# Kernel optimization log

Measured on AMD Instinct MI355X. Metric: run time of the kernel, lower is better.

Reference implementation:

```python
import jax, jax.numpy as jnp
import numpy as np

NUM_HEADS = 16
HIDDEN = 1024
HEAD = HIDDEN // NUM_HEADS
NEG_INF = -10000.0


def setup_inputs() -> dict:
    key = jax.random.key(0)
    k1, k2, k3, k4 = jax.random.split(key, 4)
    B, S = 4, 2048
    x = jax.random.normal(k1, (B, S, HIDDEN), dtype=jnp.float32)
    pos_embeds = jax.random.normal(k2, (S, HIDDEN), dtype=jnp.float32)
    # Dense(3*hidden, use_bias=False) and Dense(hidden, use_bias=False)
    Wqkv = jax.random.normal(k3, (HIDDEN, 3 * HIDDEN), dtype=jnp.float32) / np.sqrt(HIDDEN)
    Wo = jax.random.normal(k4, (HIDDEN, HIDDEN), dtype=jnp.float32) / np.sqrt(HIDDEN)
    return {"x": x, "pos_embeds": pos_embeds, "Wqkv": Wqkv, "Wo": Wo}


def _compute_qkv(t, Wqkv):
    # rearrange '... s (k n h) -> k ... n s h', k=3, n=NUM_HEADS
    proj = t @ Wqkv  # [..., s, 3*n*h]
    proj = proj.reshape(*t.shape[:-1], 3, NUM_HEADS, HEAD)  # [..., s, 3, n, h]
    # move: k first, then leading dims, then n, s, h
    nd = proj.ndim
    perm = (nd - 3,) + tuple(range(nd - 4)) + (nd - 2, nd - 4, nd - 1)
    return jnp.transpose(proj, perm)  # [3, ..., n, s, h]


def reference(x, pos_embeds, Wqkv, Wo):
    S = x.shape[-2]
    q, k, v = _compute_qkv(x, Wqkv)  # each [B, n, S, h]
    pos_qkv = _compute_qkv(pos_embeds[:S], Wqkv)  # [3, n, S, h]
    pos_q, pos_k = pos_qkv[0], pos_qkv[1]
    q = q + pos_q  # broadcast over batch
    k = k + pos_k
    scores = jnp.einsum('bnqh,bnkh->bnqk', q, k) / np.sqrt(HEAD).astype(np.float32)
    causal = jnp.arange(S)[:, None] < jnp.arange(S)[None, :]  # strict upper triangle (future)
    scores = jnp.where(causal, NEG_INF, scores)
    probs = jax.nn.softmax(scores, axis=-1)
    # dropout deterministic (training=False) -> identity
    combined = jnp.einsum('bnqk,bnkh->bnqh', probs, v)  # [B, n, S, h]
    combined = jnp.transpose(combined, (0, 2, 1, 3)).reshape(x.shape[0], S, HIDDEN)  # '... n q h -> ... q (n h)'
    out = combined @ Wo
    return out
```

## Files before the change

### kernel.cpp

```cpp
#include <hip/hip_runtime.h>


typedef float f32x4 __attribute__((ext_vector_type(4)));
typedef short bf16x8 __attribute__((ext_vector_type(8)));
typedef short bf16x4 __attribute__((ext_vector_type(4)));

#define MFMA_BF16(a, b, c) __builtin_amdgcn_mfma_f32_16x16x32_bf16((a), (b), (c), 0, 0, 0)

#if __has_builtin(__builtin_amdgcn_mfma_f32_16x16x16bf16_1k)
#define HAVE_MFMA16 1
#define MFMA_BF16_K16(a, b, c) __builtin_amdgcn_mfma_f32_16x16x16bf16_1k((a), (b), (c), 0, 0, 0)
#else
#define HAVE_MFMA16 0
#endif

__device__ __forceinline__ short f2bf(float f) {
  union { float f; unsigned u; } v; v.f = f;
  unsigned u = v.u;
  u += 0x7fffu + ((u >> 16) & 1u);
  return (short)(u >> 16);
}

__device__ __forceinline__ float bf2f(short s) {
  union { unsigned u; float f; } v;
  v.u = ((unsigned)(unsigned short)s) << 16;
  return v.f;
}

__device__ __forceinline__ float fast_exp2(float x) {
#if __has_builtin(__builtin_amdgcn_exp2f)
  return __builtin_amdgcn_exp2f(x);
#else
  return exp2f(x);
#endif
}

__device__ __forceinline__ int cvt_pk_bf16(float lo, float hi) {
  int r;
  asm("v_cvt_pk_bf16_f32 %0, %1, %2" : "=v"(r) : "v"(lo), "v"(hi));
  return r;
}

__device__ __forceinline__ void gl_lds16(const short* g, short* l) {
  __builtin_amdgcn_global_load_lds(
      (const __attribute__((address_space(1))) unsigned*)(g),
      (__attribute__((address_space(3))) unsigned*)(l), 16, 0, 0);
}

__device__ __forceinline__ int swzK(int row, int colbyte) {
  return row * 64 + (((colbyte) ^ ((row & 7) << 4)) >> 1);
}
__device__ __forceinline__ int swz32(int row, int colbyte) {
  return row * 32 + (((colbyte) ^ ((row & 3) << 4)) >> 1);
}
__device__ __forceinline__ int swzV(int row, int colbyte) {
  return row * 64 + ((((colbyte >> 3) + row) & 15) << 2);
}
__device__ __forceinline__ int swzE(int row, int col) {
  return row * 128 + ((((col >> 3) ^ (row & 15)) << 3) | (col & 7));
}

__device__ const int QT_X[30] = {5,6,7,8,9,10,11,11,12,12,13,13,14,14,15,15,
                                 4,10, 3,9,15, 2,8,14, 1,7,13, 0,6,12};
__device__ const int CH_X[30] = {0,0,0,0,0,0,0,1,0,1,0,1,0,1,0,1,
                                 0,1, 0,1,2, 0,1,2, 0,1,2, 0,1,2};
__device__ const int START_QT[16] = {0,1,2,3,4,5,6,8,10,12,14,16,18,21,24,27};

__global__ __launch_bounds__(256) void prep_and_transpose(
    const float* __restrict__ x, const float* __restrict__ pos,
    const float* __restrict__ wqkv, const float* __restrict__ wo,
    short* __restrict__ xb, short* __restrict__ xpb,
    short* __restrict__ outqkv, short* __restrict__ outo) {
  __shared__ float tile[32][33];
  const int n = blockIdx.x;
  if (n < 8192) {
    int i = n * 256 + threadIdx.x;
    int idx = i * 4;
    const float4 xv = *(const float4*)(x + idx);
    const float4 pv = *(const float4*)(pos + (idx & ((2048 * 1024) - 1)));
    short4 a, b;
    a.x = f2bf(xv.x); a.y = f2bf(xv.y); a.z = f2bf(xv.z); a.w = f2bf(xv.w);
    b.x = f2bf(xv.x + pv.x); b.y = f2bf(xv.y + pv.y);
    b.z = f2bf(xv.z + pv.z); b.w = f2bf(xv.w + pv.w);
    *(short4*)(xb + idx) = a;
    *(short4*)(xpb + idx) = b;
    return;
  }
  const int m = n - 8192;
  const int bx = m & 127;
  const int k0 = (m >> 7) * 32;
  const float* __restrict__ in = (bx < 96) ? wqkv : wo;
  short* __restrict__ out = (bx < 96) ? outqkv : outo;
  const int N = (bx < 96) ? 3072 : 1024;
  const int n0 = ((bx < 96) ? bx : (bx - 96)) * 32;
  int c = threadIdx.x & 31, r0 = threadIdx.x >> 5;
  for (int i = 0; i < 4; i++) {
    int r = r0 + i * 8;
    tile[r][c] = in[(size_t)(k0 + r) * N + n0 + c];
  }
  __syncthreads();
  for (int i = 0; i < 4; i++) {
    int r = r0 + i * 8;
    out[(size_t)(n0 + r) * 1024 + k0 + c] = f2bf(tile[c][r]);
  }
}

__global__ __launch_bounds__(256) void gemm_qkv(const short* __restrict__ xb,
                                                const short* __restrict__ xpb,
                                                const short* __restrict__ wt,
                                                short* __restrict__ qg,
                                                short* __restrict__ kg,
                                                short* __restrict__ vtg) {
  __shared__ __align__(16) short Sh[16384];
  const int n = blockIdx.x;
  const int idx = n >> 3;
  const int bm = (n & 7) * 8 + (idx & 7);
  const int bn = idx >> 3;
  const short* __restrict__ A = (bn < 16) ? xpb : xb;
  const int tid = threadIdx.x;
  const int lane = tid & 63, wid = tid >> 6;
  const int wm = wid & 1, wn = wid >> 1;
  const int quad = lane >> 4, l16 = lane & 15;
  const f32x4 fzero = {0.f, 0.f, 0.f, 0.f};
  f32x4 acc[4][4];
  for (int mt = 0; mt < 4; mt++)
    for (int nt = 0; nt < 4; nt++) acc[mt][nt] = fzero;
  const int arow0 = bm * 128, brow0 = bn * 128;

  int prow[2], pcol[2], pbase[2];
#pragma unroll
  for (int i = 0; i < 2; i++) {
    int p = (wid * 2 + i) * 64 + lane;
    prow[i] = p >> 2;
    pcol[i] = ((p & 3) ^ ((p >> 2) & 3)) * 8;
    pbase[i] = (wid * 2 + i) * 512;
  }

#define STAGE_QKV(BUF, K0)                                                    \
  {                                                                           \
    _Pragma("unroll")                                                         \
    for (int i = 0; i < 2; i++) {                                             \
      gl_lds16(A + (size_t)(arow0 + prow[i]) * 1024 + (K0) + pcol[i],         \
               Sh + (BUF)*8192 + pbase[i]);                                   \
      gl_lds16(wt + (size_t)(brow0 + prow[i]) * 1024 + (K0) + pcol[i],        \
               Sh + (BUF)*8192 + 4096 + pbase[i]);                            \
    }                                                                         \
  }

#define COMPUTE_QKV(BASE)                                                     \
  {                                                                           \
    const short* As_ = (BASE);                                                \
    const short* Bs_ = (BASE) + 4096;                                         \
    bf16x8 af[4], bfr[4];                                                     \
    _Pragma("unroll")                                                         \
    for (int mt = 0; mt < 4; mt++)                                            \
      af[mt] = *(const bf16x8*)(As_ + swz32(wm * 64 + mt * 16 + l16, quad * 16)); \
    _Pragma("unroll")                                                         \
    for (int nt = 0; nt < 4; nt++)                                            \
      bfr[nt] = *(const bf16x8*)(Bs_ + swz32(wn * 64 + nt * 16 + l16, quad * 16)); \
    _Pragma("unroll")                                                         \
    for (int mt = 0; mt < 4; mt++)                                            \
      _Pragma("unroll")                                                       \
      for (int nt = 0; nt < 4; nt++)                                          \
        acc[mt][nt] = MFMA_BF16(af[mt], bfr[nt], acc[mt][nt]);                \
  }

  STAGE_QKV(0, 0);
  __syncthreads();
  for (int t = 0; t < 32; t += 2) {
    if (t + 1 < 32) STAGE_QKV(1, (t + 1) * 32);
    COMPUTE_QKV(Sh);
    __syncthreads();
    if (t + 2 < 32) STAGE_QKV(0, (t + 2) * 32);
    COMPUTE_QKV(Sh + 8192);
    __syncthreads();
  }

  short* Sf = Sh;
  const int kk = bn >> 3;
  const int bglob = (bm * 128) >> 11;
  const int s0v = (bm * 128) & 2047;
  if (kk == 2) {
#pragma unroll
    for (int mt = 0; mt < 4; mt++)
#pragma unroll
      for (int nt = 0; nt < 4; nt++) {
        int col = wn * 64 + nt * 16 + l16;
        int sb = wm * 64 + mt * 16 + quad * 4;
        int2 pk;
        pk.x = cvt_pk_bf16(acc[mt][nt][0], acc[mt][nt][1]);
        pk.y = cvt_pk_bf16(acc[mt][nt][2], acc[mt][nt][3]);
        *(int2*)(Sf + swzE(col, sb)) = pk;
      }
    __syncthreads();
    const int col = tid >> 1, half = tid & 1;
    int head = (bn * 2 + (col >> 6)) & 15;
    int hh = col & 63;
    int4* dst = (int4*)(vtg + (size_t)((bglob * 16 + head) * 64 + hh) * 2048 + s0v + half * 64);
#pragma unroll
    for (int c = 0; c < 8; c++)
      dst[c] = *(const int4*)(Sf + swzE(col, half * 64 + c * 8));
  } else {
    const float scale = (kk == 0) ? 0.18033688f : 1.0f;
#pragma unroll
    for (int mt = 0; mt < 4; mt++)
#pragma unroll
      for (int nt = 0; nt < 4; nt++) {
        int col = wn * 64 + nt * 16 + l16;
#pragma unroll
        for (int r = 0; r < 4; r++) {
          int s_loc = wm * 64 + mt * 16 + quad * 4 + r;
          Sf[swzE(s_loc, col)] = f2bf(acc[mt][nt][r] * scale);
        }
      }
    __syncthreads();
    const int row = tid >> 1, half = tid & 1;
    int head = (bn * 2 + half) & 15;
    short* __restrict__ dstp = (kk == 0) ? qg : kg;
    int4* dst = (int4*)(dstp + (size_t)((bglob * 16 + head) * 2048 + s0v + row) * 64);
#pragma unroll
    for (int c = 0; c < 8; c++)
      dst[c] = *(const int4*)(Sf + swzE(row, half * 64 + c * 8));
  }
}

__global__ __launch_bounds__(256, 3) void attn_part(const short* __restrict__ qg,
                                                    const short* __restrict__ kg,
                                                    const short* __restrict__ vtg,
                                                    short* __restrict__ pO,
                                                    float* __restrict__ pL) {
  const int n = blockIdx.x;
  const int i = n >> 3;
  const int bh = (n & 7) * 8 + i / 30;
  const int slot = i % 30;
  const int qt = QT_X[slot], ch = CH_X[slot];
  const int p = bh * 30 + START_QT[qt] + ch;
  const short* __restrict__ Q = qg + (size_t)bh * 2048 * 64;
  const short* __restrict__ K = kg + (size_t)bh * 2048 * 64;
  const short* __restrict__ VT = vtg + (size_t)bh * 64 * 2048;
  __shared__ __align__(16) short KV[2][64 * 64];
  short* Ks = &KV[0][0];
  short* Vs = &KV[1][0];
#if !HAVE_MFMA16
  __shared__ __align__(16) short Ps[4][16 * 72];
#endif
  const int tid = threadIdx.x, lane = tid & 63, w = tid >> 6;
  const int quad = lane >> 4, l16 = lane & 15;
  const f32x4 fzero = {0.f, 0.f, 0.f, 0.f};

  bf16x8 bq[2][2];
#pragma unroll
  for (int sub = 0; sub < 2; sub++) {
    int qrow = qt * 128 + w * 32 + sub * 16 + l16;
#pragma unroll
    for (int ks = 0; ks < 2; ks++)
      bq[sub][ks] = *(const bf16x8*)(Q + (size_t)qrow * 64 + ks * 32 + quad * 8);
  }
  f32x4 acco[2][4];
  f32x4 lrun[2];
#pragma unroll
  for (int sub = 0; sub < 2; sub++) {
    for (int nt = 0; nt < 4; nt++) acco[sub][nt] = fzero;
    lrun[sub] = fzero;
  }

  const int kt0 = ch * 12;
  const int kt1 = min(kt0 + 12, 2 * qt + 2);
  const int qmin_w = qt * 128 + w * 32;

  const int sr0 = tid >> 3, sr1 = sr0 + 32;
  const int scs = (tid & 7) * 8;
  const int scb = (tid & 7) * 16;
  const int oK0 = swzK(sr0, scb), oK1 = swzK(sr1, scb);
  const int oV0a = swzV(sr0, scb), oV0b = swzV(sr0, scb + 8);
  const int oV1a = swzV(sr1, scb), oV1b = swzV(sr1, scb + 8);

  int4 kreg[2], vreg[2];
  {
    int kv0 = kt0 * 64;
    kreg[0] = *(const int4*)(K + (size_t)(kv0 + sr0) * 64 + scs);
    kreg[1] = *(const int4*)(K + (size_t)(kv0 + sr1) * 64 + scs);
    vreg[0] = *(const int4*)(VT + (size_t)sr0 * 2048 + kv0 + scs);
    vreg[1] = *(const int4*)(VT + (size_t)sr1 * 2048 + kv0 + scs);
  }

  for (int kt = kt0; kt < kt1; kt++) {
    if (kt > kt0) __syncthreads();
    *(int4*)(&Ks[oK0]) = kreg[0];
    *(int4*)(&Ks[oK1]) = kreg[1];
    *(int2*)(&Vs[oV0a]) = make_int2(vreg[0].x, vreg[0].y);
    *(int2*)(&Vs[oV0b]) = make_int2(vreg[0].z, vreg[0].w);
    *(int2*)(&Vs[oV1a]) = make_int2(vreg[1].x, vreg[1].y);
    *(int2*)(&Vs[oV1b]) = make_int2(vreg[1].z, vreg[1].w);
    __syncthreads();

    if (kt + 1 < kt1) {
      int kv0 = (kt + 1) * 64;
      kreg[0] = *(const int4*)(K + (size_t)(kv0 + sr0) * 64 + scs);
      kreg[1] = *(const int4*)(K + (size_t)(kv0 + sr1) * 64 + scs);
      vreg[0] = *(const int4*)(VT + (size_t)sr0 * 2048 + kv0 + scs);
      vreg[1] = *(const int4*)(VT + (size_t)sr1 * 2048 + kv0 + scs);
    }

    if (kt * 64 <= qmin_w + 31) {
      f32x4 accs[2][4];
#pragma unroll
      for (int sub = 0; sub < 2; sub++)
        for (int nt = 0; nt < 4; nt++) accs[sub][nt] = fzero;
      __builtin_amdgcn_s_setprio(1);
#pragma unroll
      for (int ks = 0; ks < 2; ks++)
#pragma unroll
        for (int nt = 0; nt < 4; nt++) {
          bf16x8 ak = *(const bf16x8*)(&Ks[swzK(nt * 16 + l16, ks * 64 + quad * 16)]);
          accs[0][nt] = MFMA_BF16(ak, bq[0][ks], accs[0][nt]);
          accs[1][nt] = MFMA_BF16(ak, bq[1][ks], accs[1][nt]);
        }
      __builtin_amdgcn_s_setprio(0);

      if ((kt + 1) * 64 > qmin_w) {
#pragma unroll
        for (int sub = 0; sub < 2; sub++) {
          int q = qmin_w + sub * 16 + l16;
#pragma unroll
          for (int nt = 0; nt < 4; nt++) {
            int kv = kt * 64 + nt * 16 + quad * 4;
#pragma unroll
            for (int r = 0; r < 4; r++)
              if (kv + r > q) accs[sub][nt][r] = -1e30f;
          }
        }
      }

#pragma unroll
      for (int sub = 0; sub < 2; sub++)
#pragma unroll
        for (int nt = 0; nt < 4; nt++) {
#pragma unroll
          for (int r = 0; r < 4; r++) accs[sub][nt][r] = fast_exp2(accs[sub][nt][r]);
          lrun[sub] += accs[sub][nt];
        }

#if HAVE_MFMA16
      __builtin_amdgcn_s_setprio(1);
#pragma unroll
      for (int kkk = 0; kkk < 4; kkk++) {
        union { int2 i2; bf16x4 v; } p0, p1;
        p0.i2.x = cvt_pk_bf16(accs[0][kkk][0], accs[0][kkk][1]);
        p0.i2.y = cvt_pk_bf16(accs[0][kkk][2], accs[0][kkk][3]);
        p1.i2.x = cvt_pk_bf16(accs[1][kkk][0], accs[1][kkk][1]);
        p1.i2.y = cvt_pk_bf16(accs[1][kkk][2], accs[1][kkk][3]);
#pragma unroll
        for (int nth = 0; nth < 4; nth++) {
          bf16x4 av = *(const bf16x4*)(&Vs[swzV(nth * 16 + l16, kkk * 32 + quad * 8)]);
          acco[0][nth] = MFMA_BF16_K16(av, p0.v, acco[0][nth]);
          acco[1][nth] = MFMA_BF16_K16(av, p1.v, acco[1][nth]);
        }
      }
      __builtin_amdgcn_s_setprio(0);
#else
      short* P = Ps[w];
#pragma unroll
      for (int sub = 0; sub < 2; sub++) {
#pragma unroll
        for (int nt = 0; nt < 4; nt++) {
          int2 pk;
          pk.x = cvt_pk_bf16(accs[sub][nt][0], accs[sub][nt][1]);
          pk.y = cvt_pk_bf16(accs[sub][nt][2], accs[sub][nt][3]);
          *(int2*)(P + l16 * 72 + nt * 16 + quad * 4) = pk;
        }
#pragma unroll
        for (int ks2 = 0; ks2 < 2; ks2++) {
          bf16x8 bp = *(const bf16x8*)(P + l16 * 72 + ks2 * 32 + quad * 8);
#pragma unroll
          for (int nth = 0; nth < 4; nth++) {
            int r = nth * 16 + l16;
            int4 t4;
            *(int2*)&t4.x = *(const int2*)(&Vs[swzV(r, ks2 * 64 + quad * 16)]);
            *(int2*)&t4.z = *(const int2*)(&Vs[swzV(r, ks2 * 64 + quad * 16 + 8)]);
            bf16x8 av = *(const bf16x8*)&t4;
            acco[sub][nth] = MFMA_BF16(av, bp, acco[sub][nth]);
          }
        }
      }
#endif
    }
  }

#pragma unroll
  for (int sub = 0; sub < 2; sub++) {
    float lh = (lrun[sub][0] + lrun[sub][1]) + (lrun[sub][2] + lrun[sub][3]);
    lh += __shfl_xor(lh, 16);
    lh += __shfl_xor(lh, 32);
    int qloc = w * 32 + sub * 16 + l16;
    if (quad == 0) pL[p * 128 + qloc] = lh;
  }

  __syncthreads();
  short* Ob = &KV[0][0];
#pragma unroll
  for (int sub = 0; sub < 2; sub++) {
    int qloc = w * 32 + sub * 16 + l16;
#pragma unroll
    for (int nth = 0; nth < 4; nth++) {
      int2 pk;
      pk.x = cvt_pk_bf16(acco[sub][nth][0], acco[sub][nth][1]);
      pk.y = cvt_pk_bf16(acco[sub][nth][2], acco[sub][nth][3]);
      *(int2*)(Ob + swzK(qloc, nth * 32 + quad * 8)) = pk;
    }
  }
  __syncthreads();
  {
    const int row = tid >> 1;
    const int hb = (tid & 1) * 64;
    int4 v0 = *(const int4*)(Ob + swzK(row, hb));
    int4 v1 = *(const int4*)(Ob + swzK(row, hb + 16));
    int4 v2 = *(const int4*)(Ob + swzK(row, hb + 32));
    int4 v3 = *(const int4*)(Ob + swzK(row, hb + 48));
    int4* dst = (int4*)(pO + (size_t)p * 8192 + tid * 32);
    dst[0] = v0; dst[1] = v1; dst[2] = v2; dst[3] = v3;
  }
}

__global__ __launch_bounds__(256) void attn_merge(const short* __restrict__ pO,
                                                  const float* __restrict__ pL,
                                                  short* __restrict__ comb) {
  const int n = blockIdx.x;
  const int i = n >> 3;
  const int bh = (n & 7) * 8 + (i >> 4);
  const int qt = i & 15;
  const int head = bh & 15, b = bh >> 4;
  const int nch = (2 * qt + 13) / 12;
  const int p0 = bh * 30 + START_QT[qt];
  const int t = threadIdx.x;
  const int qloc = t >> 1, hh = (t & 1) * 32;

  float l = 0.f;
  for (int c = 0; c < nch; c++) l += pL[(p0 + c) * 128 + qloc];
  const float inv = 1.f / l;

  float acc[32];
#pragma unroll
  for (int j = 0; j < 32; j++) acc[j] = 0.f;
  for (int c = 0; c < nch; c++) {
    const short* src = pO + (size_t)(p0 + c) * 8192 + (size_t)qloc * 64 + hh;
#pragma unroll
    for (int v = 0; v < 4; v++) {
      short4 d0 = *(const short4*)(src + v * 8);
      short4 d1 = *(const short4*)(src + v * 8 + 4);
      acc[v * 8 + 0] += bf2f(d0.x); acc[v * 8 + 1] += bf2f(d0.y);
      acc[v * 8 + 2] += bf2f(d0.z); acc[v * 8 + 3] += bf2f(d0.w);
      acc[v * 8 + 4] += bf2f(d1.x); acc[v * 8 + 5] += bf2f(d1.y);
      acc[v * 8 + 6] += bf2f(d1.z); acc[v * 8 + 7] += bf2f(d1.w);
    }
  }
  size_t base = (size_t)(b * 2048 + qt * 128 + qloc) * 1024 + head * 64 + hh;
#pragma unroll
  for (int v = 0; v < 8; v++) {
    short4 sv;
    sv.x = f2bf(acc[v * 4 + 0] * inv);
    sv.y = f2bf(acc[v * 4 + 1] * inv);
    sv.z = f2bf(acc[v * 4 + 2] * inv);
    sv.w = f2bf(acc[v * 4 + 3] * inv);
    *(short4*)(comb + base + v * 4) = sv;
  }
}

__global__ __launch_bounds__(256) void gemm_out(const short* __restrict__ A,
                                                const short* __restrict__ wt,
                                                float* __restrict__ out) {
  __shared__ __align__(16) short Sh[16384];
  const int n = blockIdx.x;
  const int idx = n >> 3;
  const int bm = (n & 7) * 8 + (idx & 7);
  const int bn = idx >> 3;
  const int tid = threadIdx.x;
  const int lane = tid & 63, wid = tid >> 6;
  const int wm = wid & 1, wn = wid >> 1;
  const int quad = lane >> 4, l16 = lane & 15;
  const f32x4 fzero = {0.f, 0.f, 0.f, 0.f};
  f32x4 acc[4][4];
  for (int mt = 0; mt < 4; mt++)
    for (int nt = 0; nt < 4; nt++) acc[mt][nt] = fzero;
  const int arow0 = bm * 128, brow0 = bn * 128;

  int prow[2], pcol[2], pbase[2];
#pragma unroll
  for (int i = 0; i < 2; i++) {
    int p = (wid * 2 + i) * 64 + lane;
    prow[i] = p >> 2;
    pcol[i] = ((p & 3) ^ ((p >> 2) & 3)) * 8;
    pbase[i] = (wid * 2 + i) * 512;
  }

#define STAGE_OUT(BUF, K0)                                                    \
  {                                                                           \
    _Pragma("unroll")                                                         \
    for (int i = 0; i < 2; i++) {                                             \
      gl_lds16(A + (size_t)(arow0 + prow[i]) * 1024 + (K0) + pcol[i],         \
               Sh + (BUF)*8192 + pbase[i]);                                   \
      gl_lds16(wt + (size_t)(brow0 + prow[i]) * 1024 + (K0) + pcol[i],        \
               Sh + (BUF)*8192 + 4096 + pbase[i]);                            \
    }                                                                         \
  }

#define COMPUTE_OUT(BASE)                                                     \
  {                                                                           \
    const short* As_ = (BASE);                                                \
    const short* Bs_ = (BASE) + 4096;                                         \
    bf16x8 af[4], bfr[4];                                                     \
    _Pragma("unroll")                                                         \
    for (int mt = 0; mt < 4; mt++)                                            \
      af[mt] = *(const bf16x8*)(As_ + swz32(wm * 64 + mt * 16 + l16, quad * 16)); \
    _Pragma("unroll")                                                         \
    for (int nt = 0; nt < 4; nt++)                                            \
      bfr[nt] = *(const bf16x8*)(Bs_ + swz32(wn * 64 + nt * 16 + l16, quad * 16)); \
    _Pragma("unroll")                                                         \
    for (int mt = 0; mt < 4; mt++)                                            \
      _Pragma("unroll")                                                       \
      for (int nt = 0; nt < 4; nt++)                                          \
        acc[mt][nt] = MFMA_BF16(af[mt], bfr[nt], acc[mt][nt]);                \
  }

  STAGE_OUT(0, 0);
  __syncthreads();
  for (int t = 0; t < 32; t += 2) {
    if (t + 1 < 32) STAGE_OUT(1, (t + 1) * 32);
    COMPUTE_OUT(Sh);
    __syncthreads();
    if (t + 2 < 32) STAGE_OUT(0, (t + 2) * 32);
    COMPUTE_OUT(Sh + 8192);
    __syncthreads();
  }

  for (int nt = 0; nt < 4; nt++) {
    int col = bn * 128 + wn * 64 + nt * 16 + l16;
    for (int mt = 0; mt < 4; mt++) {
      int rowb = bm * 128 + wm * 64 + mt * 16 + quad * 4;
      for (int r = 0; r < 4; r++)
        out[(size_t)(rowb + r) * 1024 + col] = acc[mt][nt][r];
    }
  }
}

extern "C" void kernel_launch(void* const* d_in, const int* in_sizes, int n_in,
                              void* d_out, int out_size, void* d_ws, size_t ws_size,
                              hipStream_t stream) {
  const float* x    = (const float*)d_in[0];
  const float* pos  = (const float*)d_in[1];
  const float* Wqkv = (const float*)d_in[2];
  const float* Wo   = (const float*)d_in[3];
  float* out = (float*)d_out;

  char* ws = (char*)d_ws;
  const size_t SZ = (size_t)8192 * 1024 * 2;
  short* xb    = (short*)(ws);
  short* xpb   = (short*)(ws + SZ);
  short* pO    = (short*)(ws);
  float* pL    = (float*)(ws + (size_t)1920 * 8192 * 2);
  short* q     = (short*)(ws + 2 * SZ);
  short* k     = (short*)(ws + 3 * SZ);
  short* vt    = (short*)(ws + 4 * SZ);
  short* comb  = (short*)(ws + 5 * SZ);
  short* wqkvt = (short*)(ws + 6 * SZ);
  short* wot   = (short*)(ws + 6 * SZ + (size_t)3072 * 1024 * 2);

  prep_and_transpose<<<dim3(12288), 256, 0, stream>>>(x, pos, Wqkv, Wo,
                                                      xb, xpb, wqkvt, wot);
  gemm_qkv<<<dim3(1536), 256, 0, stream>>>(xb, xpb, wqkvt, q, k, vt);
  attn_part<<<dim3(1920), 256, 0, stream>>>(q, k, vt, pO, pL);
  attn_merge<<<dim3(1024), 256, 0, stream>>>(pO, pL, comb);
  gemm_out<<<dim3(512), 256, 0, stream>>>(comb, wot, out);
}
```

Measured before the change: 275.6 us.

## Use 4-slot LDS ring with prefetch distance 2 in QKV and output GEMMs

Replaces the double-buffered K loop in both projection GEMMs with a four-slot shared-memory ring that keeps two tiles in flight. Each iteration needs only one barrier instead of two, and uses explicit vmcnt/lgkmcnt waits and a sched_barrier so LDS reads are issued before the next global-to-LDS prefetch and MFMAs run after them. The aim is to hide global load latency better and cut barrier stalls. The cost is doubled LDS per block (64 KB), which may reduce occupancy.

```diff
diff --git a/kernel.cpp b/kernel.cpp
--- a/kernel.cpp
+++ b/kernel.cpp
@@ -111,7 +111,7 @@
                                                 short* __restrict__ qg,
                                                 short* __restrict__ kg,
                                                 short* __restrict__ vtg) {
-  __shared__ __align__(16) short Sh[16384];
+  __shared__ __align__(16) short Sh[32768];
   const int n = blockIdx.x;
   const int idx = n >> 3;
   const int bm = (n & 7) * 8 + (idx & 7);
@@ -136,45 +136,64 @@
     pbase[i] = (wid * 2 + i) * 512;
   }
 
-#define STAGE_QKV(BUF, K0)                                                    \
+#define STAGE_Q(SLOT, K0)                                                     \
   {                                                                           \
     _Pragma("unroll")                                                         \
     for (int i = 0; i < 2; i++) {                                             \
       gl_lds16(A + (size_t)(arow0 + prow[i]) * 1024 + (K0) + pcol[i],         \
-               Sh + (BUF)*8192 + pbase[i]);                                   \
+               Sh + (SLOT)*8192 + pbase[i]);                                  \
       gl_lds16(wt + (size_t)(brow0 + prow[i]) * 1024 + (K0) + pcol[i],        \
-               Sh + (BUF)*8192 + 4096 + pbase[i]);                            \
+               Sh + (SLOT)*8192 + 4096 + pbase[i]);                           \
     }                                                                         \
   }
 
-#define COMPUTE_QKV(BASE)                                                     \
-  {                                                                           \
-    const short* As_ = (BASE);                                                \
-    const short* Bs_ = (BASE) + 4096;                                         \
-    bf16x8 af[4], bfr[4];                                                     \
-    _Pragma("unroll")                                                         \
-    for (int mt = 0; mt < 4; mt++)                                            \
+#define READS_Q(SLOT)                                                        \
+    const short* As_ = Sh + (SLOT) * 8192;                                   \
+    const short* Bs_ = As_ + 4096;                                           \
+    bf16x8 af[4], bfr[4];                                                    \
+    _Pragma("unroll")                                                        \
+    for (int mt = 0; mt < 4; mt++)                                           \
       af[mt] = *(const bf16x8*)(As_ + swz32(wm * 64 + mt * 16 + l16, quad * 16)); \
-    _Pragma("unroll")                                                         \
-    for (int nt = 0; nt < 4; nt++)                                            \
-      bfr[nt] = *(const bf16x8*)(Bs_ + swz32(wn * 64 + nt * 16 + l16, quad * 16)); \
-    _Pragma("unroll")                                                         \
-    for (int mt = 0; mt < 4; mt++)                                            \
-      _Pragma("unroll")                                                       \
-      for (int nt = 0; nt < 4; nt++)                                          \
-        acc[mt][nt] = MFMA_BF16(af[mt], bfr[nt], acc[mt][nt]);                \
-  }
-
-  STAGE_QKV(0, 0);
+    _Pragma("unroll")                                                        \
+    for (int nt = 0; nt < 4; nt++)                                           \
+      bfr[nt] = *(const bf16x8*)(Bs_ + swz32(wn * 64 + nt * 16 + l16, quad * 16));
+
+#define MFMAS_Q()                                                            \
+    _Pragma("unroll")                                                        \
+    for (int mt = 0; mt < 4; mt++)                                           \
+      _Pragma("unroll")                                                      \
+      for (int nt = 0; nt < 4; nt++)                                         \
+        acc[mt][nt] = MFMA_BF16(af[mt], bfr[nt], acc[mt][nt]);
+
+  STAGE_Q(0, 0);
+  STAGE_Q(1, 32);
+  asm volatile("s_waitcnt vmcnt(4)" ::: "memory");
+  __builtin_amdgcn_s_barrier();
+
+  for (int kt = 0; kt < 30; ++kt) {
+    READS_Q(kt & 3)
+    STAGE_Q((kt + 2) & 3, (kt + 2) * 32);
+    asm volatile("s_waitcnt vmcnt(4)" ::: "memory");
+    __builtin_amdgcn_s_barrier();
+    asm volatile("s_waitcnt lgkmcnt(0)" ::: "memory");
+    __builtin_amdgcn_sched_barrier(0);
+    MFMAS_Q()
+  }
+  {
+    READS_Q(2)
+    asm volatile("s_waitcnt vmcnt(0)" ::: "memory");
+    __builtin_amdgcn_s_barrier();
+    asm volatile("s_waitcnt lgkmcnt(0)" ::: "memory");
+    __builtin_amdgcn_sched_barrier(0);
+    MFMAS_Q()
+  }
+  {
+    READS_Q(3)
+    asm volatile("s_waitcnt lgkmcnt(0)" ::: "memory");
+    __builtin_amdgcn_sched_barrier(0);
+    MFMAS_Q()
+  }
   __syncthreads();
-  for (int t = 0; t < 32; t += 2) {
-    if (t + 1 < 32) STAGE_QKV(1, (t + 1) * 32);
-    COMPUTE_QKV(Sh);
-    __syncthreads();
-    if (t + 2 < 32) STAGE_QKV(0, (t + 2) * 32);
-    COMPUTE_QKV(Sh + 8192);
-    __syncthreads();
-  }
 
   short* Sf = Sh;
   const int kk = bn >> 3;
@@ -222,6 +241,9 @@
     for (int c = 0; c < 8; c++)
       dst[c] = *(const int4*)(Sf + swzE(row, half * 64 + c * 8));
   }
+#undef STAGE_Q
+#undef READS_Q
+#undef MFMAS_Q
 }
 
 __global__ __launch_bounds__(256, 3) void attn_part(const short* __restrict__ qg,
@@ -469,7 +491,7 @@
 __global__ __launch_bounds__(256) void gemm_out(const short* __restrict__ A,
                                                 const short* __restrict__ wt,
                                                 float* __restrict__ out) {
-  __shared__ __align__(16) short Sh[16384];
+  __shared__ __align__(16) short Sh[32768];
   const int n = blockIdx.x;
   const int idx = n >> 3;
   const int bm = (n & 7) * 8 + (idx & 7);
@@ -493,44 +515,62 @@
     pbase[i] = (wid * 2 + i) * 512;
   }
 
-#define STAGE_OUT(BUF, K0)                                                    \
+#define STAGE_O(SLOT, K0)                                                     \
   {                                                                           \
     _Pragma("unroll")                                                         \
     for (int i = 0; i < 2; i++) {                                             \
       gl_lds16(A + (size_t)(arow0 + prow[i]) * 1024 + (K0) + pcol[i],         \
-               Sh + (BUF)*8192 + pbase[i]);                                   \
+               Sh + (SLOT)*8192 + pbase[i]);                                  \
       gl_lds16(wt + (size_t)(brow0 + prow[i]) * 1024 + (K0) + pcol[i],        \
-               Sh + (BUF)*8192 + 4096 + pbase[i]);                            \
+               Sh + (SLOT)*8192 + 4096 + pbase[i]);                           \
     }                                                                         \
   }
 
-#define COMPUTE_OUT(BASE)                                                     \
-  {                                                                           \
-    const short* As_ = (BASE);                                                \
-    const short* Bs_ = (BASE) + 4096;                                         \
-    bf16x8 af[4], bfr[4];                                                     \
-    _Pragma("unroll")                                                         \
-    for (int mt = 0; mt < 4; mt++)                                            \
+#define READS_O(SLOT)                                                        \
+    const short* As_ = Sh + (SLOT) * 8192;                                   \
+    const short* Bs_ = As_ + 4096;                                           \
+    bf16x8 af[4], bfr[4];                                                    \
+    _Pragma("unroll")                                                        \
+    for (int mt = 0; mt < 4; mt++)                                           \
       af[mt] = *(const bf16x8*)(As_ + swz32(wm * 64 + mt * 16 + l16, quad * 16)); \
-    _Pragma("unroll")                                                         \
-    for (int nt = 0; nt < 4; nt++)                                            \
-      bfr[nt] = *(const bf16x8*)(Bs_ + swz32(wn * 64 + nt * 16 + l16, quad * 16)); \
-    _Pragma("unroll")                                                         \
-    for (int mt = 0; mt < 4; mt++)                                            \
-      _Pragma("unroll")                                                       \
-      for (int nt = 0; nt < 4; nt++)                                          \
-        acc[mt][nt] = MFMA_BF16(af[mt], bfr[nt], acc[mt][nt]);                \
-  }
-
-  STAGE_OUT(0, 0);
-  __syncthreads();
-  for (int t = 0; t < 32; t += 2) {
-    if (t + 1 < 32) STAGE_OUT(1, (t + 1) * 32);
-    COMPUTE_OUT(Sh);
-    __syncthreads();
-    if (t + 2 < 32) STAGE_OUT(0, (t + 2) * 32);
-    COMPUTE_OUT(Sh + 8192);
-    __syncthreads();
+    _Pragma("unroll")                                                        \
+    for (int nt = 0; nt < 4; nt++)                                           \
+      bfr[nt] = *(const bf16x8*)(Bs_ + swz32(wn * 64 + nt * 16 + l16, quad * 16));
+
+#define MFMAS_O()                                                            \
+    _Pragma("unroll")                                                        \
+    for (int mt = 0; mt < 4; mt++)                                           \
+      _Pragma("unroll")                                                      \
+      for (int nt = 0; nt < 4; nt++)                                         \
+        acc[mt][nt] = MFMA_BF16(af[mt], bfr[nt], acc[mt][nt]);
+
+  STAGE_O(0, 0);
+  STAGE_O(1, 32);
+  asm volatile("s_waitcnt vmcnt(4)" ::: "memory");
+  __builtin_amdgcn_s_barrier();
+
+  for (int kt = 0; kt < 30; ++kt) {
+    READS_O(kt & 3)
+    STAGE_O((kt + 2) & 3, (kt + 2) * 32);
+    asm volatile("s_waitcnt vmcnt(4)" ::: "memory");
+    __builtin_amdgcn_s_barrier();
+    asm volatile("s_waitcnt lgkmcnt(0)" ::: "memory");
+    __builtin_amdgcn_sched_barrier(0);
+    MFMAS_O()
+  }
+  {
+    READS_O(2)
+    asm volatile("s_waitcnt vmcnt(0)" ::: "memory");
+    __builtin_amdgcn_s_barrier();
+    asm volatile("s_waitcnt lgkmcnt(0)" ::: "memory");
+    __builtin_amdgcn_sched_barrier(0);
+    MFMAS_O()
+  }
+  {
+    READS_O(3)
+    asm volatile("s_waitcnt lgkmcnt(0)" ::: "memory");
+    __builtin_amdgcn_sched_barrier(0);
+    MFMAS_O()
   }
 
   for (int nt = 0; nt < 4; nt++) {
@@ -541,6 +581,9 @@
         out[(size_t)(rowb + r) * 1024 + col] = acc[mt][nt][r];
     }
   }
+#undef STAGE_O
+#undef READS_O
+#undef MFMAS_O
 }
 
 extern "C" void kernel_launch(void* const* d_in, const int* in_sizes, int n_in,
```

Measured after the change: 280.8 us. No clear change (+1.9%).
